# Performance work log

Measured on AMD Instinct MI355X. Metric: run time of the kernel, lower is better.

The kernel has to match this reference:

```python
import jax, jax.numpy as jnp
import numpy as np

EPS = 1e-7      # GENConv message epsilon
BN_EPS = 1e-5   # torch BatchNorm1d eps


def _genconv(x, src, dst, n, w1, b1, gamma, beta, w2, b2):
    # GENConv(aggr='softmax_sg', t=1.0): msg = relu(x_j)+eps, per-feature
    # scatter-softmax weights (stop-grad), weighted sum, residual, MLP
    # [Linear -> BatchNorm(train stats) -> ReLU -> Linear].
    msg = jnp.maximum(x[src], 0.0) + EPS                         # [E, d]
    m = jax.ops.segment_max(msg, dst, num_segments=n)            # [N, d]
    e = jnp.exp(msg - m[dst])
    s = jax.ops.segment_sum(e, dst, num_segments=n)
    alpha = jax.lax.stop_gradient(e / (s[dst] + 1e-16))          # softmax_sg
    agg = jax.ops.segment_sum(msg * alpha, dst, num_segments=n)  # [N, d]
    h = agg + x
    h = h @ w1 + b1
    mu = jnp.mean(h, axis=0)
    var = jnp.var(h, axis=0)
    h = (h - mu) * jax.lax.rsqrt(var + BN_EPS) * gamma + beta
    h = jnp.maximum(h, 0.0)
    return h @ w2 + b2


def _forward(x, edge_index, batch, target,
             g1_w1, g1_b1, g1_g, g1_be, g1_w2, g1_b2,
             g2_w1, g2_b1, g2_g, g2_be, g2_w2, g2_b2,
             g3_w1, g3_b1, g3_g, g3_be, g3_w2, g3_b2,
             fg1_w, fg1_b, fg2_w, fg2_b, fg3_w, fg3_b,
             emb, cw, cb, fxt_w, fxt_b,
             f1_w, f1_b, f2_w, f2_b, o_w, o_b):
    n = x.shape[0]
    nb = target.shape[0]
    src, dst = edge_index[0], edge_index[1]
    h = jnp.maximum(_genconv(x, src, dst, n, g1_w1, g1_b1, g1_g, g1_be, g1_w2, g1_b2), 0.0)
    h = jnp.maximum(_genconv(h, src, dst, n, g2_w1, g2_b1, g2_g, g2_be, g2_w2, g2_b2), 0.0)
    h = jnp.maximum(_genconv(h, src, dst, n, g3_w1, g3_b1, g3_g, g3_be, g3_w2, g3_b2), 0.0)
    # global mean pool over graphs
    sums = jax.ops.segment_sum(h, batch, num_segments=nb)
    cnt = jax.ops.segment_sum(jnp.ones((n, 1), h.dtype), batch, num_segments=nb)
    xg = sums / jnp.maximum(cnt, 1.0)
    xg = jnp.maximum(xg @ fg1_w + fg1_b, 0.0)
    xg = jnp.maximum(xg @ fg2_w + fg2_b, 0.0)
    xg = jnp.maximum(xg @ fg3_w + fg3_b, 0.0)
    # protein branch: embed [B,1000,128], Conv1d(1000->32,k=8) over embed axis
    ext = emb[target]                                            # [B, 1000, 128]
    conv = jax.lax.conv_general_dilated(
        ext, cw, (1,), 'VALID',
        dimension_numbers=('NCW', 'OIW', 'NCW')) + cb[None, :, None]  # [B, 32, 121]
    xt = conv.reshape(nb, 32 * 121) @ fxt_w + fxt_b
    xc = jnp.concatenate([xg, xt], axis=1)                       # [B, 256]
    xc = jnp.maximum(xc @ f1_w + f1_b, 0.0)
    xc = jnp.maximum(xc @ f2_w + f2_b, 0.0)
    return xc @ o_w + o_b


def _lin(k, i, o):
    kw, kb = jax.random.split(k)
    s = 1.0 / np.sqrt(i)
    return (jax.random.uniform(kw, (i, o), jnp.float32, -s, s),
            jax.random.uniform(kb, (o,), jnp.float32, -s, s))


def setup_inputs():
    key = jax.random.key(0)
    ks = jax.random.split(key, 32)
    N, E, B, D = 30000, 150000, 256, 78
    d = {}
    d['x'] = jax.random.normal(ks[0], (N, D), jnp.float32)
    d['edge_index'] = jax.random.randint(ks[1], (2, E), 0, N)
    d['batch'] = jnp.sort(jax.random.randint(ks[2], (N,), 0, B))
    d['target'] = jax.random.randint(ks[3], (B, 1000), 0, 26)
    dims = [(78, 156, 78), (78, 156, 312), (312, 624, 624)]
    for li, (i, hdim, o) in enumerate(dims, start=1):
        w1, b1 = _lin(ks[4 + 2 * li], i, hdim)
        w2, b2 = _lin(ks[5 + 2 * li], hdim, o)
        d['g%d_w1' % li], d['g%d_b1' % li] = w1, b1
        d['g%d_g' % li] = jnp.ones((hdim,), jnp.float32)
        d['g%d_be' % li] = jnp.zeros((hdim,), jnp.float32)
        d['g%d_w2' % li], d['g%d_b2' % li] = w2, b2
    d['fg1_w'], d['fg1_b'] = _lin(ks[14], 624, 512)
    d['fg2_w'], d['fg2_b'] = _lin(ks[15], 512, 1024)
    d['fg3_w'], d['fg3_b'] = _lin(ks[16], 1024, 128)
    d['emb'] = jax.random.normal(ks[17], (26, 128), jnp.float32)
    s = 1.0 / np.sqrt(1000 * 8)
    d['cw'] = jax.random.uniform(ks[18], (32, 1000, 8), jnp.float32, -s, s)
    d['cb'] = jax.random.uniform(ks[19], (32,), jnp.float32, -s, s)
    d['fxt_w'], d['fxt_b'] = _lin(ks[20], 32 * 121, 128)
    d['f1_w'], d['f1_b'] = _lin(ks[21], 256, 1024)
    d['f2_w'], d['f2_b'] = _lin(ks[22], 1024, 512)
    d['o_w'], d['o_b'] = _lin(ks[23], 512, 1)
    return d


def reference(x, edge_index, batch, target,
              g1_w1, g1_b1, g1_g, g1_be, g1_w2, g1_b2,
              g2_w1, g2_b1, g2_g, g2_be, g2_w2, g2_b2,
              g3_w1, g3_b1, g3_g, g3_be, g3_w2, g3_b2,
              fg1_w, fg1_b, fg2_w, fg2_b, fg3_w, fg3_b,
              emb, cw, cb, fxt_w, fxt_b,
              f1_w, f1_b, f2_w, f2_b, o_w, o_b):
    return _forward(x, edge_index, batch, target,
                    g1_w1, g1_b1, g1_g, g1_be, g1_w2, g1_b2,
                    g2_w1, g2_b1, g2_g, g2_be, g2_w2, g2_b2,
                    g3_w1, g3_b1, g3_g, g3_be, g3_w2, g3_b2,
                    fg1_w, fg1_b, fg2_w, fg2_b, fg3_w, fg3_b,
                    emb, cw, cb, fxt_w, fxt_b,
                    f1_w, f1_b, f2_w, f2_b, o_w, o_b)
```

## Files before the change

kernel.cpp:

```cpp
#include <hip/hip_runtime.h>
#include <hip/hip_bf16.h>

typedef unsigned short u16;
typedef __attribute__((ext_vector_type(8))) short bh8;
typedef __attribute__((ext_vector_type(4))) float f32x4;

static __device__ __forceinline__ float b2fu(u16 u) {
    union { float f; unsigned int i; } x;
    x.i = ((unsigned int)u) << 16;
    return x.f;
}
static __device__ __forceinline__ u16 f2bu(float f) {
    __hip_bfloat16 h = __float2bfloat16(f);
    union { __hip_bfloat16 h; u16 u; } x;
    x.h = h;
    return x.u;
}
static __device__ __forceinline__ void load2(const float* p, float& v0, float& v1) {
    float2 v = *reinterpret_cast<const float2*>(p);
    v0 = v.x; v1 = v.y;
}
static __device__ __forceinline__ void load2(const u16* p, float& v0, float& v1) {
    unsigned int u = *reinterpret_cast<const unsigned int*>(p);
    v0 = b2fu((u16)(u & 0xffff)); v1 = b2fu((u16)(u >> 16));
}

static __device__ __forceinline__ void gload16(const u16* g, u16* l) {
    __builtin_amdgcn_global_load_lds(
        (const __attribute__((address_space(1))) unsigned int*)(const void*)g,
        (__attribute__((address_space(3))) unsigned int*)(void*)l, 16, 0, 0);
}


__global__ __launch_bounds__(256) void const_out_kernel(float* __restrict__ out, float v, int n) {
    int i = blockIdx.x * 256 + threadIdx.x;
    if (i < n) out[i] = v;
}


__global__ __launch_bounds__(256) void hist_kernel(const int* __restrict__ dst,
                                                   int* __restrict__ hist, int E) {
    int e = blockIdx.x * 256 + threadIdx.x;
    if (e < E) atomicAdd(&hist[dst[e]], 1);
}

__global__ __launch_bounds__(256) void scan_kernel(const int* __restrict__ hist,
                                                   int* __restrict__ rowptr,
                                                   int* __restrict__ fill, int N) {
    __shared__ int csum[256];
    __shared__ int coff[257];
    int t = threadIdx.x;
    int chunk = (N + 255) / 256;
    int lo = min(t * chunk, N), hi = min(lo + chunk, N);
    int s = 0;
    for (int i = lo; i < hi; i++) s += hist[i];
    csum[t] = s;
    __syncthreads();
    if (t == 0) {
        int acc = 0;
        for (int i = 0; i < 256; i++) { coff[i] = acc; acc += csum[i]; }
        rowptr[N] = acc;
    }
    __syncthreads();
    int run = coff[t];
    for (int i = lo; i < hi; i++) {
        rowptr[i] = run;
        fill[i] = run;
        run += hist[i];
    }
}

__global__ __launch_bounds__(256) void scan_tiles(const int* __restrict__ hist, int N,
                                                  int* __restrict__ rowptr,
                                                  int* __restrict__ tsum) {
    int tid = threadIdx.x;
    int i = blockIdx.x * 256 + tid;
    int v = (i < N) ? hist[i] : 0;
    __shared__ int s[256];
    s[tid] = v;
    __syncthreads();
    for (int off = 1; off < 256; off <<= 1) {
        int t = (tid >= off) ? s[tid - off] : 0;
        __syncthreads();
        s[tid] += t;
        __syncthreads();
    }
    if (i < N) rowptr[i] = s[tid] - v;
    if (tid == 255) tsum[blockIdx.x] = s[255];
}

__global__ __launch_bounds__(256) void scan_tsum(const int* __restrict__ tsum, int ntiles,
                                                 int* __restrict__ toff,
                                                 int* __restrict__ totalp) {
    int tid = threadIdx.x;
    int v = (tid < ntiles) ? tsum[tid] : 0;
    __shared__ int s[256];
    s[tid] = v;
    __syncthreads();
    for (int off = 1; off < 256; off <<= 1) {
        int t = (tid >= off) ? s[tid - off] : 0;
        __syncthreads();
        s[tid] += t;
        __syncthreads();
    }
    if (tid < ntiles) toff[tid] = s[tid] - v;
    if (tid == 255) *totalp = s[255];
}

__global__ __launch_bounds__(256) void scan_apply(int* __restrict__ rowptr,
                                                  const int* __restrict__ toff, int N,
                                                  int* __restrict__ fill) {
    int i = blockIdx.x * 256 + threadIdx.x;
    if (i < N) {
        int r = rowptr[i] + toff[blockIdx.x];
        rowptr[i] = r;
        fill[i] = r;
    }
}

__global__ __launch_bounds__(256) void scatter_kernel(const int* __restrict__ src,
                                                      const int* __restrict__ dst,
                                                      int* __restrict__ fill,
                                                      int* __restrict__ srcs, int E) {
    int e = blockIdx.x * 256 + threadIdx.x;
    if (e < E) {
        int p = atomicAdd(&fill[dst[e]], 1);
        srcs[p] = src[e];
    }
}


template <typename T>
__global__ __launch_bounds__(256) void agg_kernel(const T* __restrict__ x,
                                                  const int* __restrict__ rowptr,
                                                  const int* __restrict__ srcs,
                                                  u16* __restrict__ out, int d, int Kp, int N) {
    int n = blockIdx.y * 4 + (threadIdx.x >> 6);
    int f = (blockIdx.x * 64 + (threadIdx.x & 63)) * 2;
    if (n >= N || f >= Kp) return;
    size_t o = (size_t)n * Kp + f;
    if (f >= d) {
        *reinterpret_cast<unsigned int*>(out + o) = 0;
        return;
    }
    int e0 = rowptr[n], e1 = rowptr[n + 1];
    float s0 = 0.f, t0 = 0.f, s1 = 0.f, t1 = 0.f;
    for (int e = e0; e < e1; e++) {
        int sr = srcs[e];
        float v0, v1;
        load2(x + (size_t)sr * d + f, v0, v1);
        float m0 = fmaxf(v0, 0.f) + 1e-7f;
        float w0 = __expf(m0);
        s0 += w0; t0 += m0 * w0;
        float m1 = fmaxf(v1, 0.f) + 1e-7f;
        float w1 = __expf(m1);
        s1 += w1; t1 += m1 * w1;
    }
    float x0, x1;
    load2(x + (size_t)n * d + f, x0, x1);
    float a0 = t0 / (s0 + 1e-16f) + x0;
    float a1 = t1 / (s1 + 1e-16f) + x1;
    unsigned int pk = (unsigned int)f2bu(a0) | ((unsigned int)f2bu(a1) << 16);
    *reinterpret_cast<unsigned int*>(out + o) = pk;
}


struct WtJobs {
    const float* W[6];
    u16* WT[6];
    int K[6], N[6], Kp[6], Np[6];
};

__global__ __launch_bounds__(256) void wt_cvt6(WtJobs jb) {
    int jz = blockIdx.z;
    int Kp = jb.Kp[jz], Np = jb.Np[jz];
    int n = blockIdx.y * 4 + (threadIdx.x >> 6);
    int k = blockIdx.x * 64 + (threadIdx.x & 63);
    if (n >= Np || k >= Kp) return;
    int K = jb.K[jz], N = jb.N[jz];
    float v = (n < N && k < K) ? jb.W[jz][(size_t)k * N + n] : 0.f;
    jb.WT[jz][(size_t)n * Kp + k] = f2bu(v);
}


template <int AMODE, int EMODE, bool RELU, typename CT>
__global__ __launch_bounds__(256) void gemm_mfma(const u16* __restrict__ A,
                                                 const u16* __restrict__ BT,
                                                 const float* __restrict__ bias,
                                                 CT* __restrict__ C, int ldc, int M, int Ncols,
                                                 int Kp, int kLen, int nbx, int nby, int spx,
                                                 const float* __restrict__ scale,
                                                 const float* __restrict__ shift,
                                                 float* __restrict__ osum,
                                                 float* __restrict__ osumsq) {
    int xcd = blockIdx.x & 7;
    int j = blockIdx.x >> 3;
    int bx = j % nbx;
    int by = xcd * spx + j / nbx;
    if (by >= nby) return;
    __shared__ u16 As[2][128 * 32];
    __shared__ u16 Bs[2][128 * 32];
    const int tid = threadIdx.x;
    const int lane = tid & 63;
    const int w = tid >> 6;
    const int bm = by * 128;
    const int bn = bx * 128;
    const int kw = blockIdx.y * kLen;
    f32x4 acc[4][4] = {};

    const int r0 = w * 16 + (lane >> 2);
    const int r1 = r0 + 64;
    const int sw = ((lane & 3) ^ ((r0 >> 1) & 3)) << 3;
    const u16* Ag0 = A + (size_t)(bm + r0) * Kp + sw + kw;
    const u16* Ag1 = A + (size_t)(bm + r1) * Kp + sw + kw;
    const u16* Bg0 = BT + (size_t)(bn + r0) * Kp + sw + kw;
    const u16* Bg1 = BT + (size_t)(bn + r1) * Kp + sw + kw;
    const int wb = w << 9;

    uint4 a0r, a1r;
    auto stageB = [&](int b, int koff) {
        gload16(Bg0 + koff, &Bs[b][wb]);
        gload16(Bg1 + koff, &Bs[b][2048 + wb]);
    };
    auto stageA_lds = [&](int b, int koff) {
        gload16(Ag0 + koff, &As[b][wb]);
        gload16(Ag1 + koff, &As[b][2048 + wb]);
    };
    auto loadA_reg = [&](int koff) {
        a0r = *reinterpret_cast<const uint4*>(Ag0 + koff);
        a1r = *reinterpret_cast<const uint4*>(Ag1 + koff);
    };
    auto writeA_reg = [&](int b, int koff) {
        int f0 = sw + kw + koff;
        float4 sc0 = *reinterpret_cast<const float4*>(scale + f0);
        float4 sc1 = *reinterpret_cast<const float4*>(scale + f0 + 4);
        float4 sh0 = *reinterpret_cast<const float4*>(shift + f0);
        float4 sh1 = *reinterpret_cast<const float4*>(shift + f0 + 4);
        auto tf2 = [](unsigned int u, float sa, float sb, float ha, float hb) {
            float h0 = b2fu((u16)(u & 0xffff)), h1 = b2fu((u16)(u >> 16));
            float v0 = fmaxf(fmaf(h0, sa, ha), 0.f);
            float v1 = fmaxf(fmaf(h1, sb, hb), 0.f);
            return (unsigned int)f2bu(v0) | ((unsigned int)f2bu(v1) << 16);
        };
        uint4 o0, o1;
        o0.x = tf2(a0r.x, sc0.x, sc0.y, sh0.x, sh0.y);
        o0.y = tf2(a0r.y, sc0.z, sc0.w, sh0.z, sh0.w);
        o0.z = tf2(a0r.z, sc1.x, sc1.y, sh1.x, sh1.y);
        o0.w = tf2(a0r.w, sc1.z, sc1.w, sh1.z, sh1.w);
        o1.x = tf2(a1r.x, sc0.x, sc0.y, sh0.x, sh0.y);
        o1.y = tf2(a1r.y, sc0.z, sc0.w, sh0.z, sh0.w);
        o1.z = tf2(a1r.z, sc1.x, sc1.y, sh1.x, sh1.y);
        o1.w = tf2(a1r.w, sc1.z, sc1.w, sh1.z, sh1.w);
        *reinterpret_cast<uint4*>(&As[b][wb + lane * 8]) = o0;
        *reinterpret_cast<uint4*>(&As[b][2048 + wb + lane * 8]) = o1;
    };

    const int fm = (w >> 1) * 64 + (lane & 15);
    const int fn = (w & 1) * 64 + (lane & 15);
    const int g = lane >> 4;
    const int ka = (g ^ ((fm >> 1) & 3)) << 3;
    const int kb = (g ^ ((fn >> 1) & 3)) << 3;

    const int nk = kLen >> 5;
    if constexpr (AMODE == 0) {
        stageA_lds(0, 0);
        stageB(0, 0);
        asm volatile("s_waitcnt vmcnt(0)" ::: "memory");
    } else {
        loadA_reg(0);
        stageB(0, 0);
        asm volatile("s_waitcnt vmcnt(0)" ::: "memory");
        writeA_reg(0, 0);
        asm volatile("s_waitcnt lgkmcnt(0)" ::: "memory");
    }
    __builtin_amdgcn_s_barrier();
    for (int k = 0; k < nk; k++) {
        const int cur = k & 1;
        if (k + 1 < nk) {
            if constexpr (AMODE == 0) stageA_lds(cur ^ 1, (k + 1) << 5);
            else loadA_reg((k + 1) << 5);
            stageB(cur ^ 1, (k + 1) << 5);
        }
        bh8 af[4], bf[4];
#pragma unroll
        for (int mt = 0; mt < 4; mt++)
            af[mt] = *reinterpret_cast<const bh8*>(&As[cur][(fm + mt * 16) * 32 + ka]);
#pragma unroll
        for (int nt = 0; nt < 4; nt++)
            bf[nt] = *reinterpret_cast<const bh8*>(&Bs[cur][(fn + nt * 16) * 32 + kb]);
        asm volatile("s_waitcnt lgkmcnt(0)" ::: "memory");
        __builtin_amdgcn_sched_barrier(0);
        __builtin_amdgcn_s_setprio(1);
#pragma unroll
        for (int mt = 0; mt < 4; mt++)
#pragma unroll
            for (int nt = 0; nt < 4; nt++)
                acc[mt][nt] = __builtin_amdgcn_mfma_f32_16x16x32_bf16(af[mt], bf[nt],
                                                                      acc[mt][nt], 0, 0, 0);
        __builtin_amdgcn_s_setprio(0);
        __builtin_amdgcn_sched_barrier(0);
        asm volatile("s_waitcnt vmcnt(0)" ::: "memory");
        if constexpr (AMODE == 1) {
            __builtin_amdgcn_sched_barrier(0);
            if (k + 1 < nk) writeA_reg(cur ^ 1, (k + 1) << 5);
            asm volatile("s_waitcnt lgkmcnt(0)" ::: "memory");
        }
        __builtin_amdgcn_s_barrier();
    }
    const int rq = (lane >> 4) * 4;
    const int cl = lane & 15;
    if constexpr (EMODE == 0) {
#pragma unroll
        for (int mt = 0; mt < 4; mt++) {
#pragma unroll
            for (int nt = 0; nt < 4; nt++) {
                int n = bn + (w & 1) * 64 + nt * 16 + cl;
                if (n >= Ncols) continue;
                float bv = bias[n];
#pragma unroll
                for (int r = 0; r < 4; r++) {
                    int m = bm + (w >> 1) * 64 + mt * 16 + rq + r;
                    if (m >= M) continue;
                    float v = acc[mt][nt][r] + bv;
                    if (RELU) v = fmaxf(v, 0.f);
                    if (sizeof(CT) == 2)
                        C[(size_t)m * ldc + n] = (CT)f2bu(v);
                    else
                        C[(size_t)m * ldc + n] = (CT)v;
                }
            }
        }
    } else if constexpr (EMODE == 1) {
        float cs[4] = {0.f, 0.f, 0.f, 0.f}, cq[4] = {0.f, 0.f, 0.f, 0.f};
#pragma unroll
        for (int nt = 0; nt < 4; nt++) {
            int n = bn + (w & 1) * 64 + nt * 16 + cl;
            if (n >= ldc) continue;
            float bv = (n < Ncols) ? bias[n] : 0.f;
#pragma unroll
            for (int mt = 0; mt < 4; mt++) {
#pragma unroll
                for (int r = 0; r < 4; r++) {
                    int m = bm + (w >> 1) * 64 + mt * 16 + rq + r;
                    if (m >= M) continue;
                    float v = (n < Ncols) ? acc[mt][nt][r] + bv : 0.f;
                    C[(size_t)m * ldc + n] = (CT)f2bu(v);
                    cs[nt] += v;
                    cq[nt] += v * v;
                }
            }
        }
        float* red = (float*)&As[0][0];
        const int slot = (w >> 1) * 4 + (lane >> 4);
#pragma unroll
        for (int nt = 0; nt < 4; nt++) {
            int nl = (w & 1) * 64 + nt * 16 + cl;
            red[nl * 8 + slot] = cs[nt];
            red[1024 + nl * 8 + slot] = cq[nt];
        }
        __syncthreads();
        if (tid < 128) {
            int n = bn + tid;
            if (n < Ncols) {
                float s = 0.f, q = 0.f;
#pragma unroll
                for (int i = 0; i < 8; i++) {
                    s += red[tid * 8 + i];
                    q += red[1024 + tid * 8 + i];
                }
                atomicAdd(&osum[n], s);
                atomicAdd(&osumsq[n], q);
            }
        }
    } else {
#pragma unroll
        for (int mt = 0; mt < 4; mt++) {
#pragma unroll
            for (int nt = 0; nt < 4; nt++) {
                int n = bn + (w & 1) * 64 + nt * 16 + cl;
                if (n >= Ncols) continue;
#pragma unroll
                for (int r = 0; r < 4; r++) {
                    int m = bm + (w >> 1) * 64 + mt * 16 + rq + r;
                    if (m >= M) continue;
                    atomicAdd((float*)&C[(size_t)m * ldc + n], acc[mt][nt][r]);
                }
            }
        }
    }
}


__global__ __launch_bounds__(256) void bn_final(const float* __restrict__ sum,
                                                const float* __restrict__ sumsq,
                                                const float* __restrict__ gamma,
                                                const float* __restrict__ beta,
                                                float* __restrict__ scale,
                                                float* __restrict__ shift, int dh, int Kp,
                                                float invN) {
    int i = blockIdx.x * 256 + threadIdx.x;
    if (i >= Kp) return;
    if (i < dh) {
        float mu = sum[i] * invN;
        float var = sumsq[i] * invN - mu * mu;
        float sc = gamma[i] / sqrtf(var + 1e-5f);
        scale[i] = sc;
        shift[i] = beta[i] - mu * sc;
    } else {
        scale[i] = 0.f;
        shift[i] = 0.f;
    }
}


__global__ __launch_bounds__(256) void pool_seg(const u16* __restrict__ h,
                                                const int* __restrict__ goff,
                                                float* __restrict__ gsum, int d) {
    int g = blockIdx.y;
    int c = threadIdx.x & 63;
    int f = blockIdx.x * 64 + c;
    int wv = threadIdx.x >> 6;
    int r0 = goff[g], r1 = goff[g + 1];
    float s = 0.f;
    if (f < d)
        for (int r = r0 + wv; r < r1; r += 4) s += b2fu(h[(size_t)r * d + f]);
    __shared__ float ls[4][64];
    ls[wv][c] = s;
    __syncthreads();
    if (wv == 0 && f < d) {
        float tot = ls[0][c] + ls[1][c] + ls[2][c] + ls[3][c];
        gsum[(size_t)g * d + f] = tot / fmaxf((float)(r1 - r0), 1.f);
    }
}


__global__ __launch_bounds__(256) void gemm_sk(const float* __restrict__ A, int lda,
                                               const float* __restrict__ B, int ldb,
                                               float* __restrict__ C, int ldc, int M, int K,
                                               int Nn, int KC) {
    __shared__ float As[16][17];
    __shared__ float Bs[16][68];
    const int tid = threadIdx.x;
    const int bn = blockIdx.x * 64;
    const int bm = blockIdx.y * 16;
    const int k0 = blockIdx.z * KC;
    const int kend = min(K, k0 + KC);
    const int tx = tid & 63;
    const int ty = tid >> 6;
    float acc[4] = {};
    const int am = bm + (tid >> 4);
    const int ak = tid & 15;
    for (int kk0 = k0; kk0 < kend; kk0 += 16) {
        {
            int k = kk0 + ak;
            As[ak][tid >> 4] = (am < M && k < kend) ? A[(size_t)am * lda + k] : 0.f;
        }
#pragma unroll
        for (int i = 0; i < 4; i++) {
            int k = kk0 + ty + 4 * i;
            Bs[ty + 4 * i][tx] = (k < kend && bn + tx < Nn) ? B[(size_t)k * ldb + bn + tx] : 0.f;
        }
        __syncthreads();
#pragma unroll
        for (int kk = 0; kk < 16; kk++) {
            float b = Bs[kk][tx];
#pragma unroll
            for (int i = 0; i < 4; i++) acc[i] = fmaf(As[kk][ty + 4 * i], b, acc[i]);
        }
        __syncthreads();
    }
    if (bn + tx < Nn) {
#pragma unroll
        for (int i = 0; i < 4; i++) {
            int m = bm + ty + 4 * i;
            if (m < M) atomicAdd(&C[(size_t)m * ldc + bn + tx], acc[i]);
        }
    }
}

__global__ __launch_bounds__(256) void bias_act(float* __restrict__ C, int ldc,
                                                const float* __restrict__ bias, int M, int Nn,
                                                int relu) {
    int idx = blockIdx.x * 256 + threadIdx.x;
    if (idx >= M * Nn) return;
    int m = idx / Nn, n = idx - m * Nn;
    float v = C[(size_t)m * ldc + n] + bias[n];
    C[(size_t)m * ldc + n] = relu ? fmaxf(v, 0.f) : v;
}

static void launch_gemm_small(const float* A, int lda, const float* B, int ldb,
                              const float* bias, float* C, int ldc, int M, int K, int Nn,
                              bool relu, hipStream_t stream) {
    int gx = (Nn + 63) / 64, gy = (M + 15) / 16;
    int tiles = gx * gy;
    int ksplit = 512 / tiles;
    if (ksplit < 1) ksplit = 1;
    int maxsplit = (K + 63) / 64;
    if (ksplit > maxsplit) ksplit = maxsplit;
    int KC = (((K + ksplit - 1) / ksplit) + 15) & ~15;
    ksplit = (K + KC - 1) / KC;
    gemm_sk<<<dim3(gx, gy, ksplit), 256, 0, stream>>>(A, lda, B, ldb, C, ldc, M, K, Nn, KC);
    bias_act<<<(M * Nn + 255) / 256, 256, 0, stream>>>(C, ldc, bias, M, Nn, relu ? 1 : 0);
}


__global__ __launch_bounds__(256) void hone_kernel(const int* __restrict__ target,
                                                   u16* __restrict__ H, int total) {
    int i = blockIdx.x * 256 + threadIdx.x;
    if (i >= total) return;
    int b = i / 1000, pos = i - b * 1000;
    int t = target[i];
    H[((size_t)b * 26 + t) * 1024 + pos] = 0x3F80;
}

__global__ __launch_bounds__(256) void cwt_cvt(const float* __restrict__ cw,
                                               u16* __restrict__ BT) {
    int n = blockIdx.y;
    int kk = blockIdx.x * 256 + threadIdx.x;
    int o = n >> 3, k = n & 7;
    float v = (kk < 1000) ? cw[(size_t)o * 8000 + (size_t)kk * 8 + k] : 0.f;
    BT[(size_t)n * 1024 + kk] = f2bu(v);
}

__global__ __launch_bounds__(256) void prot_conv_kernel(const float* __restrict__ S,
                                                        const float* __restrict__ emb,
                                                        const float* __restrict__ cb,
                                                        float* __restrict__ out) {
    int b = blockIdx.x;
    int tid = threadIdx.x;
    __shared__ float Sl[6656];
    __shared__ float el[26 * 128];
    for (int i = tid; i < 6656; i += 256) Sl[i] = S[(size_t)b * 6656 + i];
    for (int i = tid; i < 26 * 128; i += 256) el[i] = emb[i];
    __syncthreads();
    for (int j = tid; j < 3872; j += 256) {
        int o = j / 121;
        int w = j - o * 121;
        float acc = cb[o];
        for (int t = 0; t < 26; t++) {
#pragma unroll
            for (int k = 0; k < 8; k++)
                acc = fmaf(Sl[t * 256 + o * 8 + k], el[t * 128 + w + k], acc);
        }
        out[(size_t)b * 3872 + j] = acc;
    }
}


__global__ __launch_bounds__(256) void out_kernel(const float* __restrict__ A,
                                                  const float* __restrict__ w,
                                                  const float* __restrict__ bias,
                                                  float* __restrict__ out, int M, int K) {
    int wave = threadIdx.x >> 6;
    int lane = threadIdx.x & 63;
    int r = blockIdx.x * 4 + wave;
    if (r >= M) return;
    float acc = 0.f;
    for (int k = lane; k < K; k += 64) acc += A[(size_t)r * K + k] * w[k];
    for (int off = 32; off > 0; off >>= 1) acc += __shfl_down(acc, off, 64);
    if (lane == 0) out[r] = acc + bias[0];
}


static inline int KP(int k) { return (k + 31) & ~31; }
static inline int NP(int n) { return (n + 127) & ~127; }

extern "C" void kernel_launch(void* const* d_in, const int* in_sizes, int n_in, void* d_out,
                              int out_size, void* d_ws, size_t ws_size, hipStream_t stream) {
    static const int exp_sizes[39] = {
        2340000, 300000, 30000, 256000,
        12168, 156, 156, 156, 12168, 78,
        12168, 156, 156, 156, 48672, 312,
        194688, 624, 624, 624, 389376, 624,
        319488, 512, 524288, 1024, 131072, 128,
        3328, 256000, 32, 495616, 128,
        262144, 1024, 524288, 512, 512, 1};
    int bad = (n_in != 39) ? 100 : -1;
    if (bad < 0)
        for (int i = 0; i < 39; i++)
            if (in_sizes[i] != exp_sizes[i]) { bad = i; break; }
    if (bad >= 0) {
        const_out_kernel<<<1, 256, 0, stream>>>((float*)d_out, 2048.f + 8.f * bad, out_size);
        return;
    }

    const int N = 30000, E = 150000, B = 256;
    const int Mp = 30080;
    const int nby = 235, spx = 30;
    const int ntiles = (N + 255) / 256;
    const float* x_in = (const float*)d_in[0];
    const int* ei = (const int*)d_in[1];
    const int* src = ei;
    const int* dst = ei + E;
    const int* batch = (const int*)d_in[2];
    const int* target = (const int*)d_in[3];

    char* p = (char*)d_ws;
    auto carve = [&](size_t bytes) {
        char* r = p;
        p += (bytes + 15) & ~(size_t)15;
        return r;
    };
    int* hist = (int*)carve((size_t)(N + B) * 4);
    int* ghist = hist + N;
    int* rowptr = (int*)carve((size_t)(N + 1) * 4);
    int* fill = (int*)carve((size_t)N * 4);
    int* srcs = (int*)carve((size_t)E * 4);
    int* goff = (int*)carve((size_t)(B + 1) * 4);
    int* gfill = (int*)carve((size_t)B * 4);
    int* tsum = (int*)carve(256 * 4);
    int* toff = (int*)carve(256 * 4);
    float* sum_ = (float*)carve(2 * 624 * 4);
    float* sumsq_ = sum_ + 624;
    float* scale_ = (float*)carve(640 * 4);
    float* shift_ = (float*)carve(640 * 4);
    float* zero256 = (float*)carve(256 * 4);
    float* gsum = (float*)carve((size_t)B * 624 * 4);
    float* fc1 = (float*)carve((size_t)B * 512 * 4);
    float* fc2 = (float*)carve((size_t)B * 1024 * 4);
    float* xc = (float*)carve((size_t)B * 256 * 4);
    float* fcc1 = (float*)carve((size_t)B * 1024 * 4);
    float* fcc2 = (float*)carve((size_t)B * 512 * 4);
    float* Sbuf = (float*)carve((size_t)B * 6656 * 4);
    float* convb = (float*)carve((size_t)B * 3872 * 4);
    u16* Hbuf = (u16*)carve((size_t)B * 26 * 1024 * 2);
    u16* cwT = (u16*)carve((size_t)256 * 1024 * 2);
    u16* Abf = (u16*)carve((size_t)Mp * 640 * 2);
    u16* hmidb = (u16*)carve((size_t)Mp * 640 * 2);
    u16* Lout = (u16*)carve((size_t)N * 624 * 2);
    struct Layer { int di, dh, dn, w1, b1, g, be, w2, b2; };
    const Layer L[3] = {
        {78, 156, 78, 4, 5, 6, 7, 8, 9},
        {78, 156, 312, 10, 11, 12, 13, 14, 15},
        {312, 624, 624, 16, 17, 18, 19, 20, 21},
    };
    u16* WT1[3];
    u16* WT2[3];
    for (int li = 0; li < 3; li++) {
        WT1[li] = (u16*)carve((size_t)NP(L[li].dh) * KP(L[li].di) * 2);
        WT2[li] = (u16*)carve((size_t)NP(L[li].dn) * KP(L[li].dh) * 2);
    }
    size_t need = (size_t)(p - (char*)d_ws);
    if (ws_size < need) {
        const_out_kernel<<<1, 256, 0, stream>>>((float*)d_out,
                                                1024.f + (float)(ws_size >> 20), out_size);
        return;
    }

    hipMemsetAsync(hist, 0, (size_t)(N + B) * 4, stream);
    hipMemsetAsync(zero256, 0, 256 * 4, stream);
    hist_kernel<<<(E + 255) / 256, 256, 0, stream>>>(dst, hist, E);
    hist_kernel<<<(N + 255) / 256, 256, 0, stream>>>(batch, ghist, N);
    scan_tiles<<<ntiles, 256, 0, stream>>>(hist, N, rowptr, tsum);
    scan_tsum<<<1, 256, 0, stream>>>(tsum, ntiles, toff, rowptr + N);
    scan_apply<<<ntiles, 256, 0, stream>>>(rowptr, toff, N, fill);
    scan_kernel<<<1, 256, 0, stream>>>(ghist, goff, gfill, B);
    scatter_kernel<<<(E + 255) / 256, 256, 0, stream>>>(src, dst, fill, srcs, E);

    {
        WtJobs jb;
        int mgx = 1, mgy = 1;
        for (int li = 0; li < 3; li++) {
            jb.W[2 * li] = (const float*)d_in[L[li].w1];
            jb.WT[2 * li] = WT1[li];
            jb.K[2 * li] = L[li].di; jb.N[2 * li] = L[li].dh;
            jb.Kp[2 * li] = KP(L[li].di); jb.Np[2 * li] = NP(L[li].dh);
            jb.W[2 * li + 1] = (const float*)d_in[L[li].w2];
            jb.WT[2 * li + 1] = WT2[li];
            jb.K[2 * li + 1] = L[li].dh; jb.N[2 * li + 1] = L[li].dn;
            jb.Kp[2 * li + 1] = KP(L[li].dh); jb.Np[2 * li + 1] = NP(L[li].dn);
        }
        for (int i = 0; i < 6; i++) {
            int gx = (jb.Kp[i] + 63) / 64, gy = jb.Np[i] / 4;
            if (gx > mgx) mgx = gx;
            if (gy > mgy) mgy = gy;
        }
        wt_cvt6<<<dim3(mgx, mgy, 6), 256, 0, stream>>>(jb);
    }

    for (int li = 0; li < 3; li++) {
        const int di = L[li].di, dh = L[li].dh, dn = L[li].dn;
        const int Kp1 = KP(di), Kp2 = KP(dh);
        if (li == 0)
            agg_kernel<float><<<dim3((Kp1 / 2 + 63) / 64, (N + 3) / 4), 256, 0, stream>>>(
                x_in, rowptr, srcs, Abf, di, Kp1, N);
        else
            agg_kernel<u16><<<dim3((Kp1 / 2 + 63) / 64, (N + 3) / 4), 256, 0, stream>>>(
                Lout, rowptr, srcs, Abf, di, Kp1, N);
        hipMemsetAsync(sum_, 0, 2 * 624 * 4, stream);
        {
            int nbx = NP(dh) / 128;
            gemm_mfma<0, 1, false, u16><<<dim3(8 * spx * nbx), 256, 0, stream>>>(
                Abf, WT1[li], (const float*)d_in[L[li].b1], hmidb, Kp2, N, dh, Kp1, Kp1, nbx,
                nby, spx, nullptr, nullptr, sum_, sumsq_);
        }
        bn_final<<<(Kp2 + 255) / 256, 256, 0, stream>>>(
            sum_, sumsq_, (const float*)d_in[L[li].g], (const float*)d_in[L[li].be], scale_,
            shift_, dh, Kp2, 1.0f / N);
        {
            int nbx = NP(dn) / 128;
            gemm_mfma<1, 0, true, u16><<<dim3(8 * spx * nbx), 256, 0, stream>>>(
                hmidb, WT2[li], (const float*)d_in[L[li].b2], Lout, dn, N, dn, Kp2, Kp2, nbx,
                nby, spx, scale_, shift_, nullptr, nullptr);
        }
    }

    pool_seg<<<dim3(10, B), 256, 0, stream>>>(Lout, goff, gsum, 624);

    hipMemsetAsync(fc1, 0, (size_t)B * 3328 * 4, stream);

    launch_gemm_small(gsum, 624, (const float*)d_in[22], 512, (const float*)d_in[23], fc1, 512,
                      B, 624, 512, true, stream);
    launch_gemm_small(fc1, 512, (const float*)d_in[24], 1024, (const float*)d_in[25], fc2, 1024,
                      B, 512, 1024, true, stream);
    launch_gemm_small(fc2, 1024, (const float*)d_in[26], 128, (const float*)d_in[27], xc, 256,
                      B, 1024, 128, true, stream);

    hipMemsetAsync(Hbuf, 0, (size_t)B * 26 * 1024 * 2, stream);
    hipMemsetAsync(Sbuf, 0, (size_t)B * 6656 * 4, stream);
    hone_kernel<<<(B * 1000 + 255) / 256, 256, 0, stream>>>(target, Hbuf, B * 1000);
    cwt_cvt<<<dim3(4, 256), 256, 0, stream>>>((const float*)d_in[29], cwT);
    {
        int nbxS = 2, nbyS = 52, spxS = 7;
        gemm_mfma<0, 2, false, float><<<dim3(8 * spxS * nbxS, 4), 256, 0, stream>>>(
            Hbuf, cwT, zero256, Sbuf, 256, 6656, 256, 1024, 256, nbxS, nbyS, spxS, nullptr,
            nullptr, nullptr, nullptr);
    }
    prot_conv_kernel<<<B, 256, 0, stream>>>(Sbuf, (const float*)d_in[28],
                                            (const float*)d_in[30], convb);
    launch_gemm_small(convb, 3872, (const float*)d_in[31], 128, (const float*)d_in[32],
                      xc + 128, 256, B, 3872, 128, false, stream);

    launch_gemm_small(xc, 256, (const float*)d_in[33], 1024, (const float*)d_in[34], fcc1, 1024,
                      B, 256, 1024, true, stream);
    launch_gemm_small(fcc1, 1024, (const float*)d_in[35], 512, (const float*)d_in[36], fcc2, 512,
                      B, 1024, 512, true, stream);
    out_kernel<<<(B + 3) / 4, 256, 0, stream>>>(fcc2, (const float*)d_in[37],
                                                (const float*)d_in[38], (float*)d_out, B, 512);
}
```

Measured before the change: 808.9 us.

## Fuse bias/ReLU into split-K GEMMs, vectorize aggregation, merge histogram launches

Removes the separate bias_act passes. Bias is now written into every output buffer by one batched prefill kernel before the atomic split-K GEMMs, and the ReLU of each previous layer is applied when the next GEMM (or the output kernel) loads its A operand. The two histogram launches are merged into one kernel. The GNN aggregation kernel gets 4- or 8-wide bf16 loads for layers 2 and 3, which requires padding the layer outputs to a multiple-of-8 leading dimension with zero-filled columns. Together these cut launch count and widen gathers, at the cost of redundant ReLU work in the load path and more indexing complexity.

```diff
diff --git a/kernel.cpp b/kernel.cpp
--- a/kernel.cpp
+++ b/kernel.cpp
@@ -16,14 +16,6 @@
     x.h = h;
     return x.u;
 }
-static __device__ __forceinline__ void load2(const float* p, float& v0, float& v1) {
-    float2 v = *reinterpret_cast<const float2*>(p);
-    v0 = v.x; v1 = v.y;
-}
-static __device__ __forceinline__ void load2(const u16* p, float& v0, float& v1) {
-    unsigned int u = *reinterpret_cast<const unsigned int*>(p);
-    v0 = b2fu((u16)(u & 0xffff)); v1 = b2fu((u16)(u >> 16));
-}
 
 static __device__ __forceinline__ void gload16(const u16* g, u16* l) {
     __builtin_amdgcn_global_load_lds(
@@ -38,10 +30,13 @@
 }
 
 
-__global__ __launch_bounds__(256) void hist_kernel(const int* __restrict__ dst,
-                                                   int* __restrict__ hist, int E) {
-    int e = blockIdx.x * 256 + threadIdx.x;
-    if (e < E) atomicAdd(&hist[dst[e]], 1);
+__global__ __launch_bounds__(256) void hist2_kernel(const int* __restrict__ dst,
+                                                    const int* __restrict__ batch,
+                                                    int* __restrict__ hist,
+                                                    int* __restrict__ ghist, int E, int N) {
+    int i = blockIdx.x * 256 + threadIdx.x;
+    if (i < E) atomicAdd(&hist[dst[i]], 1);
+    else if (i < E + N) atomicAdd(&ghist[batch[i - E]], 1);
 }
 
 __global__ __launch_bounds__(256) void scan_kernel(const int* __restrict__ hist,
@@ -130,38 +125,78 @@
 }
 
 
-template <typename T>
+template <typename T, int VEC>
 __global__ __launch_bounds__(256) void agg_kernel(const T* __restrict__ x,
                                                   const int* __restrict__ rowptr,
                                                   const int* __restrict__ srcs,
-                                                  u16* __restrict__ out, int d, int Kp, int N) {
+                                                  u16* __restrict__ out, int d, int ldx,
+                                                  int Kp, int N) {
     int n = blockIdx.y * 4 + (threadIdx.x >> 6);
-    int f = (blockIdx.x * 64 + (threadIdx.x & 63)) * 2;
-    if (n >= N || f >= Kp) return;
-    size_t o = (size_t)n * Kp + f;
-    if (f >= d) {
-        *reinterpret_cast<unsigned int*>(out + o) = 0;
+    int f0 = (blockIdx.x * 64 + (threadIdx.x & 63)) * VEC;
+    if (n >= N || f0 >= Kp) return;
+    size_t o = (size_t)n * Kp + f0;
+    if (f0 >= d) {
+#pragma unroll
+        for (int i = 0; i < VEC; i++) out[o + i] = 0;
         return;
     }
+    auto loadV = [&](const T* row, float* v) {
+        if constexpr (sizeof(T) == 4) {
+            float2 t = *reinterpret_cast<const float2*>(row);
+            v[0] = t.x; v[1] = t.y;
+        } else if constexpr (VEC == 2) {
+            unsigned int u = *reinterpret_cast<const unsigned int*>(row);
+            v[0] = b2fu((u16)(u & 0xffff)); v[1] = b2fu((u16)(u >> 16));
+        } else if constexpr (VEC == 4) {
+            uint2 u = *reinterpret_cast<const uint2*>(row);
+            v[0] = b2fu((u16)(u.x & 0xffff)); v[1] = b2fu((u16)(u.x >> 16));
+            v[2] = b2fu((u16)(u.y & 0xffff)); v[3] = b2fu((u16)(u.y >> 16));
+        } else {
+            uint4 u = *reinterpret_cast<const uint4*>(row);
+            v[0] = b2fu((u16)(u.x & 0xffff)); v[1] = b2fu((u16)(u.x >> 16));
+            v[2] = b2fu((u16)(u.y & 0xffff)); v[3] = b2fu((u16)(u.y >> 16));
+            v[4] = b2fu((u16)(u.z & 0xffff)); v[5] = b2fu((u16)(u.z >> 16));
+            v[6] = b2fu((u16)(u.w & 0xffff)); v[7] = b2fu((u16)(u.w >> 16));
+        }
+    };
     int e0 = rowptr[n], e1 = rowptr[n + 1];
-    float s0 = 0.f, t0 = 0.f, s1 = 0.f, t1 = 0.f;
+    float s[VEC] = {}, t[VEC] = {};
     for (int e = e0; e < e1; e++) {
         int sr = srcs[e];
-        float v0, v1;
-        load2(x + (size_t)sr * d + f, v0, v1);
-        float m0 = fmaxf(v0, 0.f) + 1e-7f;
-        float w0 = __expf(m0);
-        s0 += w0; t0 += m0 * w0;
-        float m1 = fmaxf(v1, 0.f) + 1e-7f;
-        float w1 = __expf(m1);
-        s1 += w1; t1 += m1 * w1;
-    }
-    float x0, x1;
-    load2(x + (size_t)n * d + f, x0, x1);
-    float a0 = t0 / (s0 + 1e-16f) + x0;
-    float a1 = t1 / (s1 + 1e-16f) + x1;
-    unsigned int pk = (unsigned int)f2bu(a0) | ((unsigned int)f2bu(a1) << 16);
-    *reinterpret_cast<unsigned int*>(out + o) = pk;
+        float v[VEC];
+        loadV(x + (size_t)sr * ldx + f0, v);
+#pragma unroll
+        for (int i = 0; i < VEC; i++) {
+            float m = fmaxf(v[i], 0.f) + 1e-7f;
+            float wv = __expf(m);
+            s[i] += wv;
+            t[i] += m * wv;
+        }
+    }
+    float xs[VEC];
+    loadV(x + (size_t)n * ldx + f0, xs);
+    u16 ob[VEC];
+#pragma unroll
+    for (int i = 0; i < VEC; i++) {
+        float a = t[i] / (s[i] + 1e-16f) + xs[i];
+        ob[i] = (f0 + i < d) ? f2bu(a) : (u16)0;
+    }
+    if constexpr (VEC == 2) {
+        *reinterpret_cast<unsigned int*>(out + o) =
+            (unsigned int)ob[0] | ((unsigned int)ob[1] << 16);
+    } else if constexpr (VEC == 4) {
+        uint2 u;
+        u.x = (unsigned int)ob[0] | ((unsigned int)ob[1] << 16);
+        u.y = (unsigned int)ob[2] | ((unsigned int)ob[3] << 16);
+        *reinterpret_cast<uint2*>(out + o) = u;
+    } else {
+        uint4 u;
+        u.x = (unsigned int)ob[0] | ((unsigned int)ob[1] << 16);
+        u.y = (unsigned int)ob[2] | ((unsigned int)ob[3] << 16);
+        u.z = (unsigned int)ob[4] | ((unsigned int)ob[5] << 16);
+        u.w = (unsigned int)ob[6] | ((unsigned int)ob[7] << 16);
+        *reinterpret_cast<uint4*>(out + o) = u;
+    }
 }
 
 
@@ -315,13 +350,14 @@
 #pragma unroll
             for (int nt = 0; nt < 4; nt++) {
                 int n = bn + (w & 1) * 64 + nt * 16 + cl;
-                if (n >= Ncols) continue;
-                float bv = bias[n];
+                if (n >= ldc) continue;
+                bool valid = (n < Ncols);
+                float bv = valid ? bias[n] : 0.f;
 #pragma unroll
                 for (int r = 0; r < 4; r++) {
                     int m = bm + (w >> 1) * 64 + mt * 16 + rq + r;
                     if (m >= M) continue;
-                    float v = acc[mt][nt][r] + bv;
+                    float v = valid ? acc[mt][nt][r] + bv : 0.f;
                     if (RELU) v = fmaxf(v, 0.f);
                     if (sizeof(CT) == 2)
                         C[(size_t)m * ldc + n] = (CT)f2bu(v);
@@ -437,7 +473,7 @@
 __global__ __launch_bounds__(256) void gemm_sk(const float* __restrict__ A, int lda,
                                                const float* __restrict__ B, int ldb,
                                                float* __restrict__ C, int ldc, int M, int K,
-                                               int Nn, int KC) {
+                                               int Nn, int KC, int klim) {
     __shared__ float As[16][17];
     __shared__ float Bs[16][68];
     const int tid = threadIdx.x;
@@ -453,7 +489,9 @@
     for (int kk0 = k0; kk0 < kend; kk0 += 16) {
         {
             int k = kk0 + ak;
-            As[ak][tid >> 4] = (am < M && k < kend) ? A[(size_t)am * lda + k] : 0.f;
+            float v = (am < M && k < kend) ? A[(size_t)am * lda + k] : 0.f;
+            if (k < klim) v = fmaxf(v, 0.f);
+            As[ak][tid >> 4] = v;
         }
 #pragma unroll
         for (int i = 0; i < 4; i++) {
@@ -478,19 +516,9 @@
     }
 }
 
-__global__ __launch_bounds__(256) void bias_act(float* __restrict__ C, int ldc,
-                                                const float* __restrict__ bias, int M, int Nn,
-                                                int relu) {
-    int idx = blockIdx.x * 256 + threadIdx.x;
-    if (idx >= M * Nn) return;
-    int m = idx / Nn, n = idx - m * Nn;
-    float v = C[(size_t)m * ldc + n] + bias[n];
-    C[(size_t)m * ldc + n] = relu ? fmaxf(v, 0.f) : v;
-}
-
 static void launch_gemm_small(const float* A, int lda, const float* B, int ldb,
-                              const float* bias, float* C, int ldc, int M, int K, int Nn,
-                              bool relu, hipStream_t stream) {
+                              float* C, int ldc, int M, int K, int Nn, int klim,
+                              hipStream_t stream) {
     int gx = (Nn + 63) / 64, gy = (M + 15) / 16;
     int tiles = gx * gy;
     int ksplit = 512 / tiles;
@@ -499,8 +527,24 @@
     if (ksplit > maxsplit) ksplit = maxsplit;
     int KC = (((K + ksplit - 1) / ksplit) + 15) & ~15;
     ksplit = (K + KC - 1) / KC;
-    gemm_sk<<<dim3(gx, gy, ksplit), 256, 0, stream>>>(A, lda, B, ldb, C, ldc, M, K, Nn, KC);
-    bias_act<<<(M * Nn + 255) / 256, 256, 0, stream>>>(C, ldc, bias, M, Nn, relu ? 1 : 0);
+    gemm_sk<<<dim3(gx, gy, ksplit), 256, 0, stream>>>(A, lda, B, ldb, C, ldc, M, K, Nn, KC,
+                                                      klim);
+}
+
+
+struct FillJobs {
+    float* C[6];
+    const float* b[6];
+    int ld[6], n0[6], n1[6];
+};
+
+__global__ __launch_bounds__(256) void prefill6(FillJobs jb, int M) {
+    int jz = blockIdx.z;
+    int w = jb.n1[jz] - jb.n0[jz];
+    int i = blockIdx.x * 256 + threadIdx.x;
+    if (i >= M * w) return;
+    int m = i / w, n = i - m * w;
+    jb.C[jz][(size_t)m * jb.ld[jz] + jb.n0[jz] + n] = jb.b[jz][n];
 }
 
 
@@ -556,7 +600,7 @@
     int r = blockIdx.x * 4 + wave;
     if (r >= M) return;
     float acc = 0.f;
-    for (int k = lane; k < K; k += 64) acc += A[(size_t)r * K + k] * w[k];
+    for (int k = lane; k < K; k += 64) acc += fmaxf(A[(size_t)r * K + k], 0.f) * w[k];
     for (int off = 32; off > 0; off >>= 1) acc += __shfl_down(acc, off, 64);
     if (lane == 0) out[r] = acc + bias[0];
 }
@@ -564,6 +608,7 @@
 
 static inline int KP(int k) { return (k + 31) & ~31; }
 static inline int NP(int n) { return (n + 127) & ~127; }
+static inline int LD8(int n) { return (n + 7) & ~7; }
 
 extern "C" void kernel_launch(void* const* d_in, const int* in_sizes, int n_in, void* d_out,
                               int out_size, void* d_ws, size_t ws_size, hipStream_t stream) {
@@ -649,8 +694,7 @@
 
     hipMemsetAsync(hist, 0, (size_t)(N + B) * 4, stream);
     hipMemsetAsync(zero256, 0, 256 * 4, stream);
-    hist_kernel<<<(E + 255) / 256, 256, 0, stream>>>(dst, hist, E);
-    hist_kernel<<<(N + 255) / 256, 256, 0, stream>>>(batch, ghist, N);
+    hist2_kernel<<<(E + N + 255) / 256, 256, 0, stream>>>(dst, batch, hist, ghist, E, N);
     scan_tiles<<<ntiles, 256, 0, stream>>>(hist, N, rowptr, tsum);
     scan_tsum<<<1, 256, 0, stream>>>(tsum, ntiles, toff, rowptr + N);
     scan_apply<<<ntiles, 256, 0, stream>>>(rowptr, toff, N, fill);
@@ -678,15 +722,19 @@
         wt_cvt6<<<dim3(mgx, mgy, 6), 256, 0, stream>>>(jb);
     }
 
+    const int ldo[3] = {LD8(L[0].dn), LD8(L[1].dn), LD8(L[2].dn)};
     for (int li = 0; li < 3; li++) {
         const int di = L[li].di, dh = L[li].dh, dn = L[li].dn;
         const int Kp1 = KP(di), Kp2 = KP(dh);
         if (li == 0)
-            agg_kernel<float><<<dim3((Kp1 / 2 + 63) / 64, (N + 3) / 4), 256, 0, stream>>>(
-                x_in, rowptr, srcs, Abf, di, Kp1, N);
+            agg_kernel<float, 2><<<dim3((Kp1 / 2 + 63) / 64, (N + 3) / 4), 256, 0, stream>>>(
+                x_in, rowptr, srcs, Abf, di, di, Kp1, N);
+        else if (li == 1)
+            agg_kernel<u16, 4><<<dim3((Kp1 / 4 + 63) / 64, (N + 3) / 4), 256, 0, stream>>>(
+                Lout, rowptr, srcs, Abf, di, ldo[0], Kp1, N);
         else
-            agg_kernel<u16><<<dim3((Kp1 / 2 + 63) / 64, (N + 3) / 4), 256, 0, stream>>>(
-                Lout, rowptr, srcs, Abf, di, Kp1, N);
+            agg_kernel<u16, 8><<<dim3((Kp1 / 8 + 63) / 64, (N + 3) / 4), 256, 0, stream>>>(
+                Lout, rowptr, srcs, Abf, di, ldo[1], Kp1, N);
         hipMemsetAsync(sum_, 0, 2 * 624 * 4, stream);
         {
             int nbx = NP(dh) / 128;
@@ -700,21 +748,29 @@
         {
             int nbx = NP(dn) / 128;
             gemm_mfma<1, 0, true, u16><<<dim3(8 * spx * nbx), 256, 0, stream>>>(
-                hmidb, WT2[li], (const float*)d_in[L[li].b2], Lout, dn, N, dn, Kp2, Kp2, nbx,
-                nby, spx, scale_, shift_, nullptr, nullptr);
+                hmidb, WT2[li], (const float*)d_in[L[li].b2], Lout, ldo[li], N, dn, Kp2, Kp2,
+                nbx, nby, spx, scale_, shift_, nullptr, nullptr);
         }
     }
 
     pool_seg<<<dim3(10, B), 256, 0, stream>>>(Lout, goff, gsum, 624);
 
-    hipMemsetAsync(fc1, 0, (size_t)B * 3328 * 4, stream);
-
-    launch_gemm_small(gsum, 624, (const float*)d_in[22], 512, (const float*)d_in[23], fc1, 512,
-                      B, 624, 512, true, stream);
-    launch_gemm_small(fc1, 512, (const float*)d_in[24], 1024, (const float*)d_in[25], fc2, 1024,
-                      B, 512, 1024, true, stream);
-    launch_gemm_small(fc2, 1024, (const float*)d_in[26], 128, (const float*)d_in[27], xc, 256,
-                      B, 1024, 128, true, stream);
+    {
+        FillJobs fj;
+        fj.C[0] = fc1;  fj.b[0] = (const float*)d_in[23]; fj.ld[0] = 512;  fj.n0[0] = 0;   fj.n1[0] = 512;
+        fj.C[1] = fc2;  fj.b[1] = (const float*)d_in[25]; fj.ld[1] = 1024; fj.n0[1] = 0;   fj.n1[1] = 1024;
+        fj.C[2] = xc;   fj.b[2] = (const float*)d_in[27]; fj.ld[2] = 256;  fj.n0[2] = 0;   fj.n1[2] = 128;
+        fj.C[3] = xc;   fj.b[3] = (const float*)d_in[32]; fj.ld[3] = 256;  fj.n0[3] = 128; fj.n1[3] = 256;
+        fj.C[4] = fcc1; fj.b[4] = (const float*)d_in[34]; fj.ld[4] = 1024; fj.n0[4] = 0;   fj.n1[4] = 1024;
+        fj.C[5] = fcc2; fj.b[5] = (const float*)d_in[36]; fj.ld[5] = 512;  fj.n0[5] = 0;   fj.n1[5] = 512;
+        prefill6<<<dim3((B * 1024 + 255) / 256, 1, 6), 256, 0, stream>>>(fj, B);
+    }
+
+    launch_gemm_small(gsum, 624, (const float*)d_in[22], 512, fc1, 512, B, 624, 512, 0, stream);
+    launch_gemm_small(fc1, 512, (const float*)d_in[24], 1024, fc2, 1024, B, 512, 1024, 512,
+                      stream);
+    launch_gemm_small(fc2, 1024, (const float*)d_in[26], 128, xc, 256, B, 1024, 128, 1024,
+                      stream);
 
     hipMemsetAsync(Hbuf, 0, (size_t)B * 26 * 1024 * 2, stream);
     hipMemsetAsync(Sbuf, 0, (size_t)B * 6656 * 4, stream);
@@ -728,13 +784,13 @@
     }
     prot_conv_kernel<<<B, 256, 0, stream>>>(Sbuf, (const float*)d_in[28],
                                             (const float*)d_in[30], convb);
-    launch_gemm_small(convb, 3872, (const float*)d_in[31], 128, (const float*)d_in[32],
-                      xc + 128, 256, B, 3872, 128, false, stream);
-
-    launch_gemm_small(xc, 256, (const float*)d_in[33], 1024, (const float*)d_in[34], fcc1, 1024,
-                      B, 256, 1024, true, stream);
-    launch_gemm_small(fcc1, 1024, (const float*)d_in[35], 512, (const float*)d_in[36], fcc2, 512,
-                      B, 1024, 512, true, stream);
+    launch_gemm_small(convb, 3872, (const float*)d_in[31], 128, xc + 128, 256, B, 3872, 128, 0,
+                      stream);
+
+    launch_gemm_small(xc, 256, (const float*)d_in[33], 1024, fcc1, 1024, B, 256, 1024, 128,
+                      stream);
+    launch_gemm_small(fcc1, 1024, (const float*)d_in[35], 512, fcc2, 512, B, 1024, 512, 1024,
+                      stream);
     out_kernel<<<(B + 3) / 4, 256, 0, stream>>>(fcc2, (const float*)d_in[37],
                                                 (const float*)d_in[38], (float*)d_out, B, 512);
 }
```

Result: faster. 772.2 us (-4.5%).
